# Optimization experiments

Measured on AMD Instinct MI355X. Metric: run time of the kernel, lower is better.

Reference implementation:

```python
import jax, jax.numpy as jnp
import numpy as np

N = 100000   # nodes per node type
E = 600000   # edges per relation
D = 128      # feature dim == hidden_dim


def setup_inputs() -> dict:
    key = jax.random.key(0)
    ks = jax.random.split(key, 20)
    w = lambda k, shape: jax.random.normal(k, shape, dtype=jnp.float32) * (1.0 / np.sqrt(D))
    inp = {
        "x_player": jax.random.normal(ks[0], (N, D), dtype=jnp.float32),
        "x_team":   jax.random.normal(ks[1], (N, D), dtype=jnp.float32),
        "ei_pt": jax.random.randint(ks[2], (2, E), 0, N, dtype=jnp.int32),  # player -> team
        "ei_tp": jax.random.randint(ks[3], (2, E), 0, N, dtype=jnp.int32),  # team -> player
    }
    names = ["Wl0_pt", "Wr0_pt", "Wl0_tp", "Wr0_tp", "Wl1_pt", "Wr1_pt", "Wl1_tp", "Wr1_tp"]
    for i, n in enumerate(names):
        inp[n] = w(ks[4 + i], (D, D))
    for i, n in enumerate(["bl0_pt", "bl0_tp", "bl1_pt", "bl1_tp"]):
        inp[n] = w(ks[12 + i], (D,))
    return inp


def _sage(x_src, x_dst, ei, Wl, bl, Wr):
    # PyG SAGEConv(aggr='mean'): lin_l(mean-aggregated neighbor msgs) + lin_r(x_dst)
    src, dst = ei[0], ei[1]
    msg = x_src[src]                                              # [E, D] gather
    s = jax.ops.segment_sum(msg, dst, num_segments=x_dst.shape[0])
    c = jax.ops.segment_sum(jnp.ones((ei.shape[1], 1), x_src.dtype), dst,
                            num_segments=x_dst.shape[0])
    mean = s / jnp.maximum(c, 1.0)                                # isolated nodes -> 0
    return mean @ Wl.T + bl + x_dst @ Wr.T


def reference(x_player, x_team, ei_pt, ei_tp,
              Wl0_pt, bl0_pt, Wr0_pt, Wl0_tp, bl0_tp, Wr0_tp,
              Wl1_pt, bl1_pt, Wr1_pt, Wl1_tp, bl1_tp, Wr1_tp):
    # Layer 0 (HeteroConv sum: each node type receives exactly one relation)
    h_team = _sage(x_player, x_team, ei_pt, Wl0_pt, bl0_pt, Wr0_pt)
    h_player = _sage(x_team, x_player, ei_tp, Wl0_tp, bl0_tp, Wr0_tp)
    h_team = jax.nn.relu(h_team)      # dropout p=0.0 -> identity
    h_player = jax.nn.relu(h_player)
    # Layer 1 (no relu/dropout after last layer)
    o_team = _sage(h_player, h_team, ei_pt, Wl1_pt, bl1_pt, Wr1_pt)
    o_player = _sage(h_team, h_player, ei_tp, Wl1_tp, bl1_tp, Wr1_tp)
    return (o_player, o_team)
```

## Files before the change

### kernel.cpp

```cpp
#include <hip/hip_runtime.h>
#include <hip/hip_bf16.h>
#include <stdint.h>

typedef __attribute__((ext_vector_type(8))) short bf16x8;
typedef __attribute__((ext_vector_type(4))) float f32x4;
typedef __attribute__((ext_vector_type(4))) unsigned int u32x4;

__device__ __forceinline__ unsigned short f2bf(float f) {
  union { float f; unsigned int u; } c; c.f = f;
  unsigned int u = c.u;
  u += 0x7FFFu + ((u >> 16) & 1u);
  return (unsigned short)(u >> 16);
}
__device__ __forceinline__ float bf2f(unsigned short b) {
  union { unsigned int u; float f; } c; c.u = ((unsigned int)b) << 16;
  return c.f;
}
__device__ __forceinline__ void acc8(const u32x4& v, float* a) {
  a[0] += bf2f((unsigned short)(v[0] & 0xFFFF)); a[1] += bf2f((unsigned short)(v[0] >> 16));
  a[2] += bf2f((unsigned short)(v[1] & 0xFFFF)); a[3] += bf2f((unsigned short)(v[1] >> 16));
  a[4] += bf2f((unsigned short)(v[2] & 0xFFFF)); a[5] += bf2f((unsigned short)(v[2] >> 16));
  a[6] += bf2f((unsigned short)(v[3] & 0xFFFF)); a[7] += bf2f((unsigned short)(v[3] >> 16));
}

__global__ void cvt_x(const float* __restrict__ a, const float* __restrict__ b,
                      unsigned short* __restrict__ oa, unsigned short* __restrict__ ob, int n) {
  const float* src = blockIdx.y ? b : a;
  unsigned short* dst = blockIdx.y ? ob : oa;
  int i = (blockIdx.x * 256 + threadIdx.x) * 8;
  if (i >= n) return;
  float4 v0 = *(const float4*)(src + i);
  float4 v1 = *(const float4*)(src + i + 4);
  u32x4 o;
  o[0] = (unsigned int)f2bf(v0.x) | ((unsigned int)f2bf(v0.y) << 16);
  o[1] = (unsigned int)f2bf(v0.z) | ((unsigned int)f2bf(v0.w) << 16);
  o[2] = (unsigned int)f2bf(v1.x) | ((unsigned int)f2bf(v1.y) << 16);
  o[3] = (unsigned int)f2bf(v1.z) | ((unsigned int)f2bf(v1.w) << 16);
  *(u32x4*)(dst + i) = o;
}

struct WPtrs { const float* p[8]; };

__global__ void cvt_w(WPtrs w, unsigned short* __restrict__ out) {
  int wi = blockIdx.y;
  int i = (blockIdx.x * 256 + threadIdx.x) * 8;
  const float* src = w.p[wi];
  float4 v0 = *(const float4*)(src + i);
  float4 v1 = *(const float4*)(src + i + 4);
  u32x4 o;
  o[0] = (unsigned int)f2bf(v0.x) | ((unsigned int)f2bf(v0.y) << 16);
  o[1] = (unsigned int)f2bf(v0.z) | ((unsigned int)f2bf(v0.w) << 16);
  o[2] = (unsigned int)f2bf(v1.x) | ((unsigned int)f2bf(v1.y) << 16);
  o[3] = (unsigned int)f2bf(v1.z) | ((unsigned int)f2bf(v1.w) << 16);
  *(u32x4*)(out + wi * 16384 + i) = o;
}

__global__ void hist2_k(const int* __restrict__ ei0, const int* __restrict__ ei1,
                        int* __restrict__ cnt, int E, int N) {
  const int* ei = blockIdx.y ? ei1 : ei0;
  int* c = cnt + blockIdx.y * N;
  int e = blockIdx.x * 256 + threadIdx.x;
  if (e < E) atomicAdd(&c[ei[E + e]], 1);
}

__global__ void scan_a2(const int* __restrict__ cnt, int* __restrict__ incl,
                        int* __restrict__ bsum, int n) {
  const int* in = cnt + blockIdx.y * n;
  int* out = incl + blockIdx.y * n;
  int* bs = bsum + blockIdx.y * 128;
  __shared__ int sm[1024];
  int i = blockIdx.x * 1024 + threadIdx.x;
  int v = (i < n) ? in[i] : 0;
  sm[threadIdx.x] = v;
  __syncthreads();
  for (int off = 1; off < 1024; off <<= 1) {
    int t = (threadIdx.x >= off) ? sm[threadIdx.x - off] : 0;
    __syncthreads();
    sm[threadIdx.x] += t;
    __syncthreads();
  }
  if (i < n) out[i] = sm[threadIdx.x];
  if (threadIdx.x == 1023) bs[blockIdx.x] = sm[1023];
}

__global__ void scan_b2(int* __restrict__ bsum, int nb) {
  int* bs = bsum + blockIdx.y * 128;
  __shared__ int sm[128];
  int t = threadIdx.x;
  int v = (t < nb) ? bs[t] : 0;
  sm[t] = v;
  __syncthreads();
  for (int off = 1; off < 128; off <<= 1) {
    int u = (t >= off) ? sm[t - off] : 0;
    __syncthreads();
    sm[t] += u;
    __syncthreads();
  }
  if (t < nb) bs[t] = sm[t] - v;
}

__global__ void scan_c2(const int* __restrict__ cnt, const int* __restrict__ incl,
                        const int* __restrict__ bsum, int* __restrict__ rowptr,
                        int* __restrict__ cursor, int n) {
  int y = blockIdx.y;
  int i = blockIdx.x * 256 + threadIdx.x;
  if (i >= n) return;
  int e = incl[y * n + i] - cnt[y * n + i] + bsum[y * 128 + (i >> 10)];
  rowptr[y * n + i] = e;
  cursor[y * n + i] = e;
}

__global__ void reorder2_k(const int* __restrict__ ei0, const int* __restrict__ ei1,
                           int* __restrict__ cursor, int* __restrict__ ssrc, int E, int N) {
  const int* ei = blockIdx.y ? ei1 : ei0;
  int* cur = cursor + blockIdx.y * N;
  int* ss = ssrc + blockIdx.y * E;
  int e = blockIdx.x * 256 + threadIdx.x;
  if (e >= E) return;
  int s = ei[e];
  int d = ei[E + e];
  int pos = atomicAdd(&cur[d], 1);
  ss[pos] = s;
}

struct FusedArgs {
  const unsigned short* xsrc; const unsigned short* xdst;
  const int* rowptr; const int* cnt; const int* ssrc;
  const unsigned short* Wl; const unsigned short* Wr;
  const float* bias; void* out;
};

template<int RELU_BF16>
__global__ __launch_bounds__(256, 4) void fused_k(FusedArgs f0, FusedArgs f1, int n) {
  FusedArgs A = blockIdx.y ? f1 : f0;
  __shared__ unsigned short lds[2 * 64 * 136];
  int n0 = blockIdx.x * 64;
  int tid = threadIdx.x;
  int wave = tid >> 6, lane = tid & 63;
  int lr = lane & 15;
  int kb = (lane >> 4) * 8;

  {
    int g = tid >> 4;
    int q = (tid & 15) * 8;
    #pragma unroll
    for (int sweep = 0; sweep < 4; ++sweep) {
      int node = n0 + sweep * 16 + g;
      float a[8] = {0.f,0.f,0.f,0.f,0.f,0.f,0.f,0.f};
      float inv = 0.f;
      if (node < n) {
        int beg = A.rowptr[node];
        int deg = A.cnt[node];
        inv = deg > 0 ? 1.0f / (float)deg : 0.0f;
        int t = 0;
        for (; t + 4 <= deg; t += 4) {
          int s0 = A.ssrc[beg + t], s1 = A.ssrc[beg + t + 1];
          int s2 = A.ssrc[beg + t + 2], s3 = A.ssrc[beg + t + 3];
          u32x4 v0 = *(const u32x4*)(A.xsrc + (size_t)s0 * 128 + q);
          u32x4 v1 = *(const u32x4*)(A.xsrc + (size_t)s1 * 128 + q);
          u32x4 v2 = *(const u32x4*)(A.xsrc + (size_t)s2 * 128 + q);
          u32x4 v3 = *(const u32x4*)(A.xsrc + (size_t)s3 * 128 + q);
          acc8(v0, a); acc8(v1, a); acc8(v2, a); acc8(v3, a);
        }
        for (; t < deg; ++t) {
          int s = A.ssrc[beg + t];
          u32x4 v = *(const u32x4*)(A.xsrc + (size_t)s * 128 + q);
          acc8(v, a);
        }
      }
      u32x4 o;
      o[0] = (unsigned int)f2bf(a[0]*inv) | ((unsigned int)f2bf(a[1]*inv) << 16);
      o[1] = (unsigned int)f2bf(a[2]*inv) | ((unsigned int)f2bf(a[3]*inv) << 16);
      o[2] = (unsigned int)f2bf(a[4]*inv) | ((unsigned int)f2bf(a[5]*inv) << 16);
      o[3] = (unsigned int)f2bf(a[6]*inv) | ((unsigned int)f2bf(a[7]*inv) << 16);
      *(u32x4*)(lds + (sweep * 16 + g) * 136 + q) = o;
    }
  }

  {
    unsigned short* dstl = lds + 64 * 136;
    #pragma unroll
    for (int it = 0; it < 4; ++it) {
      int li = (it * 256 + tid) * 8;
      int r = li >> 7, c = li & 127;
      u32x4 v = {0u, 0u, 0u, 0u};
      int row = n0 + r;
      if (row < n) v = *(const u32x4*)(A.xdst + (size_t)row * 128 + c);
      *(u32x4*)(dstl + r * 136 + c) = v;
    }
  }

  const unsigned short* Wg[2] = { A.Wl, A.Wr };
  bf16x8 breg[2][2][4];
  #pragma unroll
  for (int h = 0; h < 2; ++h) {
    const unsigned short* wb = Wg[h] + (size_t)(wave * 32 + lr) * 128 + kb;
    #pragma unroll
    for (int jt = 0; jt < 2; ++jt)
      #pragma unroll
      for (int ks = 0; ks < 4; ++ks)
        breg[h][jt][ks] = *(const bf16x8*)(wb + jt * 16 * 128 + ks * 32);
  }
  __syncthreads();

  f32x4 acc[4][2] = {};
  #pragma unroll
  for (int h = 0; h < 2; ++h) {
    const unsigned short* Abase = lds + h * 64 * 136 + lr * 136 + kb;
    #pragma unroll
    for (int rt = 0; rt < 4; ++rt) {
      #pragma unroll
      for (int ks = 0; ks < 4; ++ks) {
        bf16x8 a = *(const bf16x8*)(Abase + rt * 16 * 136 + ks * 32);
        acc[rt][0] = __builtin_amdgcn_mfma_f32_16x16x32_bf16(a, breg[h][0][ks], acc[rt][0], 0, 0, 0);
        acc[rt][1] = __builtin_amdgcn_mfma_f32_16x16x32_bf16(a, breg[h][1][ks], acc[rt][1], 0, 0, 0);
      }
    }
  }

  #pragma unroll
  for (int jt = 0; jt < 2; ++jt) {
    int col = wave * 32 + jt * 16 + lr;
    float bv = A.bias[col];
    #pragma unroll
    for (int rt = 0; rt < 4; ++rt) {
      int rbase = n0 + rt * 16 + (lane >> 4) * 4;
      #pragma unroll
      for (int i = 0; i < 4; ++i) {
        int row = rbase + i;
        if (row < n) {
          float v = acc[rt][jt][i] + bv;
          if (RELU_BF16) {
            v = v > 0.f ? v : 0.f;
            ((unsigned short*)A.out)[(size_t)row * 128 + col] = f2bf(v);
          } else {
            ((float*)A.out)[(size_t)row * 128 + col] = v;
          }
        }
      }
    }
  }
}

extern "C" void kernel_launch(void* const* d_in, const int* in_sizes, int n_in,
                              void* d_out, int out_size, void* d_ws, size_t ws_size,
                              hipStream_t stream) {
  const float* xp = (const float*)d_in[0];
  const float* xt = (const float*)d_in[1];
  const int* ei_pt = (const int*)d_in[2];
  const int* ei_tp = (const int*)d_in[3];
  WPtrs wp;
  for (int i = 0; i < 8; ++i) wp.p[i] = (const float*)d_in[4 + i];
  const float* bl0_pt = (const float*)d_in[12];
  const float* bl0_tp = (const float*)d_in[13];
  const float* bl1_pt = (const float*)d_in[14];
  const float* bl1_tp = (const float*)d_in[15];
  float* out = (float*)d_out;

  const int N = in_sizes[0] / 128;
  const int E = in_sizes[2] / 2;
  const size_t NB = (size_t)N * 128 * 2;

  char* ws = (char*)d_ws;
  size_t off = 0;
  auto alloc = [&](size_t bytes) -> void* {
    off = (off + 255) & ~(size_t)255;
    void* p = ws + off; off += bytes; return p;
  };
  unsigned short* xp_bf  = (unsigned short*)alloc(NB);
  unsigned short* xt_bf  = (unsigned short*)alloc(NB);
  unsigned short* hp_bf  = (unsigned short*)alloc(NB);
  unsigned short* ht_bf  = (unsigned short*)alloc(NB);
  unsigned short* wbf    = (unsigned short*)alloc(8 * 16384 * 2);
  int* cnt    = (int*)alloc((size_t)2 * N * 4);
  int* rowptr = (int*)alloc((size_t)2 * N * 4);
  int* cursor = (int*)alloc((size_t)2 * N * 4);
  int* incl   = (int*)alloc((size_t)2 * N * 4);
  int* ssrc   = (int*)alloc((size_t)2 * E * 4);
  int* bsum   = (int*)alloc(2 * 128 * 4);

  const int nx = N * 128;
  cvt_x<<<dim3((nx / 8 + 255) / 256, 2), 256, 0, stream>>>(xp, xt, xp_bf, xt_bf, nx);
  cvt_w<<<dim3(8, 8), 256, 0, stream>>>(wp, wbf);

  const int SCB = (N + 1023) / 1024;
  hipMemsetAsync(cnt, 0, (size_t)2 * N * 4, stream);
  hist2_k<<<dim3((E + 255) / 256, 2), 256, 0, stream>>>(ei_pt, ei_tp, cnt, E, N);
  scan_a2<<<dim3(SCB, 2), 1024, 0, stream>>>(cnt, incl, bsum, N);
  scan_b2<<<dim3(1, 2), 128, 0, stream>>>(bsum, SCB);
  scan_c2<<<dim3((N + 255) / 256, 2), 256, 0, stream>>>(cnt, incl, bsum, rowptr, cursor, N);
  reorder2_k<<<dim3((E + 255) / 256, 2), 256, 0, stream>>>(ei_pt, ei_tp, cursor, ssrc, E, N);

  const int LNB = (N + 63) / 64;
  FusedArgs l0a = { xp_bf, xt_bf, rowptr,     cnt,     ssrc,     wbf + 0*16384, wbf + 1*16384, bl0_pt, ht_bf };
  FusedArgs l0b = { xt_bf, xp_bf, rowptr + N, cnt + N, ssrc + E, wbf + 2*16384, wbf + 3*16384, bl0_tp, hp_bf };
  fused_k<1><<<dim3(LNB, 2), 256, 0, stream>>>(l0a, l0b, N);
  FusedArgs l1a = { hp_bf, ht_bf, rowptr,     cnt,     ssrc,     wbf + 4*16384, wbf + 5*16384, bl1_pt, out + (size_t)N * 128 };
  FusedArgs l1b = { ht_bf, hp_bf, rowptr + N, cnt + N, ssrc + E, wbf + 6*16384, wbf + 7*16384, bl1_tp, out };
  fused_k<0><<<dim3(LNB, 2), 256, 0, stream>>>(l1a, l1b, N);
}
```

Baseline: 563.7 us.

## Unroll gather by eight with clamped indices and stage output through LDS

The neighbor-gather loop now issues eight index and row loads per iteration, with clamped indices and predicated accumulation, so more loads are in flight. Row pointers and degrees for all four sweeps are loaded up front. The epilogue writes results to LDS first and then stores them to global memory as coalesced 16-byte vectors, replacing the scattered scalar stores. In exchange it adds wasted loads for low-degree nodes, an extra barrier and LDS traffic, and more register pressure.

```diff
diff --git a/kernel.cpp b/kernel.cpp
--- a/kernel.cpp
+++ b/kernel.cpp
@@ -133,7 +133,7 @@
 template<int RELU_BF16>
 __global__ __launch_bounds__(256, 4) void fused_k(FusedArgs f0, FusedArgs f1, int n) {
   FusedArgs A = blockIdx.y ? f1 : f0;
-  __shared__ unsigned short lds[2 * 64 * 136];
+  __shared__ __align__(16) unsigned short lds[2 * 64 * 136];
   int n0 = blockIdx.x * 64;
   int tid = threadIdx.x;
   int wave = tid >> 6, lane = tid & 63;
@@ -143,37 +143,57 @@
   {
     int g = tid >> 4;
     int q = (tid & 15) * 8;
-    #pragma unroll
-    for (int sweep = 0; sweep < 4; ++sweep) {
-      int node = n0 + sweep * 16 + g;
+    int begs[4], degs[4];
+    #pragma unroll
+    for (int s = 0; s < 4; ++s) {
+      int nd = n0 + s * 16 + g;
+      bool ok = nd < n;
+      begs[s] = ok ? A.rowptr[nd] : 0;
+      degs[s] = ok ? A.cnt[nd] : 0;
+    }
+    #pragma unroll
+    for (int s = 0; s < 4; ++s) {
+      int beg = begs[s], deg = degs[s];
       float a[8] = {0.f,0.f,0.f,0.f,0.f,0.f,0.f,0.f};
-      float inv = 0.f;
-      if (node < n) {
-        int beg = A.rowptr[node];
-        int deg = A.cnt[node];
-        inv = deg > 0 ? 1.0f / (float)deg : 0.0f;
+      if (deg > 0) {
+        int elast = beg + deg - 1;
         int t = 0;
-        for (; t + 4 <= deg; t += 4) {
-          int s0 = A.ssrc[beg + t], s1 = A.ssrc[beg + t + 1];
-          int s2 = A.ssrc[beg + t + 2], s3 = A.ssrc[beg + t + 3];
-          u32x4 v0 = *(const u32x4*)(A.xsrc + (size_t)s0 * 128 + q);
-          u32x4 v1 = *(const u32x4*)(A.xsrc + (size_t)s1 * 128 + q);
-          u32x4 v2 = *(const u32x4*)(A.xsrc + (size_t)s2 * 128 + q);
-          u32x4 v3 = *(const u32x4*)(A.xsrc + (size_t)s3 * 128 + q);
-          acc8(v0, a); acc8(v1, a); acc8(v2, a); acc8(v3, a);
-        }
-        for (; t < deg; ++t) {
-          int s = A.ssrc[beg + t];
-          u32x4 v = *(const u32x4*)(A.xsrc + (size_t)s * 128 + q);
-          acc8(v, a);
-        }
-      }
+        do {
+          int i0 = A.ssrc[min(beg + t + 0, elast)];
+          int i1 = A.ssrc[min(beg + t + 1, elast)];
+          int i2 = A.ssrc[min(beg + t + 2, elast)];
+          int i3 = A.ssrc[min(beg + t + 3, elast)];
+          int i4 = A.ssrc[min(beg + t + 4, elast)];
+          int i5 = A.ssrc[min(beg + t + 5, elast)];
+          int i6 = A.ssrc[min(beg + t + 6, elast)];
+          int i7 = A.ssrc[min(beg + t + 7, elast)];
+          u32x4 v0 = *(const u32x4*)(A.xsrc + (size_t)i0 * 128 + q);
+          u32x4 v1 = *(const u32x4*)(A.xsrc + (size_t)i1 * 128 + q);
+          u32x4 v2 = *(const u32x4*)(A.xsrc + (size_t)i2 * 128 + q);
+          u32x4 v3 = *(const u32x4*)(A.xsrc + (size_t)i3 * 128 + q);
+          u32x4 v4 = *(const u32x4*)(A.xsrc + (size_t)i4 * 128 + q);
+          u32x4 v5 = *(const u32x4*)(A.xsrc + (size_t)i5 * 128 + q);
+          u32x4 v6 = *(const u32x4*)(A.xsrc + (size_t)i6 * 128 + q);
+          u32x4 v7 = *(const u32x4*)(A.xsrc + (size_t)i7 * 128 + q);
+          int rem = deg - t;
+          if (rem > 0) acc8(v0, a);
+          if (rem > 1) acc8(v1, a);
+          if (rem > 2) acc8(v2, a);
+          if (rem > 3) acc8(v3, a);
+          if (rem > 4) acc8(v4, a);
+          if (rem > 5) acc8(v5, a);
+          if (rem > 6) acc8(v6, a);
+          if (rem > 7) acc8(v7, a);
+          t += 8;
+        } while (t < deg);
+      }
+      float inv = deg > 0 ? 1.0f / (float)deg : 0.0f;
       u32x4 o;
       o[0] = (unsigned int)f2bf(a[0]*inv) | ((unsigned int)f2bf(a[1]*inv) << 16);
       o[1] = (unsigned int)f2bf(a[2]*inv) | ((unsigned int)f2bf(a[3]*inv) << 16);
       o[2] = (unsigned int)f2bf(a[4]*inv) | ((unsigned int)f2bf(a[5]*inv) << 16);
       o[3] = (unsigned int)f2bf(a[6]*inv) | ((unsigned int)f2bf(a[7]*inv) << 16);
-      *(u32x4*)(lds + (sweep * 16 + g) * 136 + q) = o;
+      *(u32x4*)(lds + (s * 16 + g) * 136 + q) = o;
     }
   }
 
@@ -218,25 +238,56 @@
     }
   }
 
-  #pragma unroll
-  for (int jt = 0; jt < 2; ++jt) {
-    int col = wave * 32 + jt * 16 + lr;
-    float bv = A.bias[col];
-    #pragma unroll
-    for (int rt = 0; rt < 4; ++rt) {
-      int rbase = n0 + rt * 16 + (lane >> 4) * 4;
+  __syncthreads();
+  if (RELU_BF16) {
+    unsigned short* st = (unsigned short*)lds;
+    #pragma unroll
+    for (int jt = 0; jt < 2; ++jt) {
+      int col = wave * 32 + jt * 16 + lr;
+      float bv = A.bias[col];
       #pragma unroll
-      for (int i = 0; i < 4; ++i) {
-        int row = rbase + i;
-        if (row < n) {
+      for (int rt = 0; rt < 4; ++rt) {
+        int rloc = rt * 16 + (lane >> 4) * 4;
+        #pragma unroll
+        for (int i = 0; i < 4; ++i) {
           float v = acc[rt][jt][i] + bv;
-          if (RELU_BF16) {
-            v = v > 0.f ? v : 0.f;
-            ((unsigned short*)A.out)[(size_t)row * 128 + col] = f2bf(v);
-          } else {
-            ((float*)A.out)[(size_t)row * 128 + col] = v;
-          }
+          v = v > 0.f ? v : 0.f;
+          st[(rloc + i) * 136 + col] = f2bf(v);
         }
+      }
+    }
+    __syncthreads();
+    #pragma unroll
+    for (int it = 0; it < 4; ++it) {
+      int flat = (it * 256 + tid) * 8;
+      int r = flat >> 7, c = flat & 127;
+      if (n0 + r < n) {
+        u32x4 v = *(const u32x4*)(st + r * 136 + c);
+        *(u32x4*)((unsigned short*)A.out + (size_t)(n0 + r) * 128 + c) = v;
+      }
+    }
+  } else {
+    float* st = (float*)lds;
+    #pragma unroll
+    for (int jt = 0; jt < 2; ++jt) {
+      int col = wave * 32 + jt * 16 + lr;
+      float bv = A.bias[col];
+      #pragma unroll
+      for (int rt = 0; rt < 4; ++rt) {
+        int rloc = rt * 16 + (lane >> 4) * 4;
+        #pragma unroll
+        for (int i = 0; i < 4; ++i)
+          st[(rloc + i) * 132 + col] = acc[rt][jt][i] + bv;
+      }
+    }
+    __syncthreads();
+    #pragma unroll
+    for (int it = 0; it < 8; ++it) {
+      int flat = (it * 256 + tid) * 4;
+      int r = flat >> 7, c = flat & 127;
+      if (n0 + r < n) {
+        u32x4 v = *(const u32x4*)(st + r * 132 + c);
+        *(u32x4*)((float*)A.out + (size_t)(n0 + r) * 128 + c) = v;
       }
     }
   }
```

After: 503.9 us. -10.6%, faster.
